# Optimization experiments

Measured on AMD Instinct MI355X. Metric: run time of the kernel, lower is better.

## Reference

```python
import jax, jax.numpy as jnp
import numpy as np

R = 5                       # kernels_radius
D = 2 * R + 1               # kernels_diameter
KERNELS_DESC = [
    {"weight": 0.9, "xy": 6.0, "image": 0.1},
    {"weight": 0.1, "xy": 6.0},
]


def _unfold(t, r):
    """torch F.unfold with padding=r, stride=1 -> [N, C, D, D, H, W]."""
    N, C, H, W = t.shape
    d = 2 * r + 1
    tp = jnp.pad(t, ((0, 0), (0, 0), (r, r), (r, r)))
    # fixed small loop over D*D kernel offsets (121), not over data dims
    pats = jnp.stack(
        [tp[:, :, i:i + H, j:j + W] for i in range(d) for j in range(d)],
        axis=2,
    )
    return pats.reshape(N, C, d, d, H, W)


def reference(x, y_hat):
    N, _, H, W = x.shape
    dt = x.dtype
    # xy coordinate feature [N, 2, H, W]: (col index, row index)
    cols = jnp.broadcast_to(jnp.arange(W, dtype=dt)[None, :], (H, W))
    rows = jnp.broadcast_to(jnp.arange(H, dtype=dt)[:, None], (H, W))
    xy = jnp.broadcast_to(jnp.stack([cols, rows], 0)[None], (N, 2, H, W))

    kernels = jnp.zeros((N, 1, D, D, H, W), dtype=dt)
    for desc in KERNELS_DESC:
        feats = []
        for modality, sigma in desc.items():
            if modality == 'weight':
                continue
            f = xy if modality == 'xy' else x
            feats.append(f / sigma)
        features = jnp.concatenate(feats, axis=1)          # [N, c, H, W]
        k = _unfold(features, R)                           # [N, c, D, D, H, W]
        k = k - k[:, :, R, R][:, :, None, None]            # diff to window center
        k = jnp.exp((-0.5 * k ** 2).sum(axis=1, keepdims=True))
        k = k.at[:, :, R, R].set(0.0)                      # zero self-affinity
        kernels = kernels + desc['weight'] * k

    Cy = y_hat.shape[1]
    yu = _unfold(y_hat, R)                                  # [N, Cy, D, D, H, W]
    prod = (kernels * yu).reshape(N, Cy, D * D, H, W).sum(axis=2)
    loss = kernels.sum() - (prod * y_hat).sum()
    denom = jnp.asarray(N * H * W, dtype=dt)
    return loss / denom


def setup_inputs() -> dict:
    key = jax.random.key(0)
    k1, k2 = jax.random.split(key)
    x = jax.random.normal(k1, (4, 3, 128, 128), dtype=jnp.float32)
    y_hat = jax.random.uniform(k2, (4, 21, 128, 128), dtype=jnp.float32)
    return {"x": x, "y_hat": y_hat}
```

## Files before the change

### kernel.cpp

```cpp
#include <hip/hip_runtime.h>

typedef _Float16 half2_t __attribute__((ext_vector_type(2)));

constexpr int IMG_H = 128;
constexpr int IMG_W = 128;
constexpr int N_IMG = 4;
constexpr int CXCH = 3;
constexpr int CYCH = 21;
constexpr int RAD = 5;
constexpr int DIA = 11;
constexpr int TILE_H = 8;
constexpr int TILE_W = 16;
constexpr int PT_H = TILE_H + 2 * RAD;
constexpr int PT_W = TILE_W + 2 * RAD;
constexpr int NPIX = PT_H * PT_W;
constexpr int NPIXT = TILE_H * TILE_W;
constexpr int NGROUP = 4;
constexpr int NTHREADS = NPIXT * NGROUP;
constexpr int NPAIR = 60;
constexpr int PPG = NPAIR / NGROUP;
constexpr int HW = IMG_H * IMG_W;
constexpr int SYW = 12;


__device__ __forceinline__ unsigned pkh(float a, float b) {
    half2_t h; h.x = (_Float16)a; h.y = (_Float16)b;
    unsigned u; __builtin_memcpy(&u, &h, 4); return u;
}
__device__ __forceinline__ half2_t uph(unsigned u) {
    half2_t h; __builtin_memcpy(&h, &u, 4); return h;
}
__device__ __forceinline__ float dot2(unsigned a, half2_t b, float c) {
#if __has_builtin(__builtin_amdgcn_fdot2)
    return __builtin_amdgcn_fdot2(uph(a), b, c, false);
#else
    half2_t ah = uph(a);
    return c + (float)ah.x * (float)b.x + (float)ah.y * (float)b.y;
#endif
}

__global__ __launch_bounds__(NTHREADS, 4)
void gcrf_kernel(const float* __restrict__ x, const float* __restrict__ y,
                 float* __restrict__ out) {
    __shared__ __align__(16) unsigned syh[NPIX * SYW];
    __shared__ int   s_pk[NPAIR];
    __shared__ float s_e1[NPAIR];
    __shared__ float s_red[NTHREADS / 64];

    const int tid = threadIdx.x;
    const int n = blockIdx.z;
    const int h0 = blockIdx.y * TILE_H;
    const int w0 = blockIdx.x * TILE_W;

    const float* xb = x + (size_t)n * CXCH * HW;
    const float* yb = y + (size_t)n * CYCH * HW;

    if (tid < NPAIR) {
        int di = tid < 5 ? 0 : 1 + (tid - 5) / 11;
        int dj = tid < 5 ? tid + 1 : (tid - 5) % 11 - 5;
        s_pk[tid] = (di << 8) | (dj + 8);
        s_e1[tid] = __expf(-0.5f * (float)(di * di + dj * dj) * (1.0f / 36.0f));
    }

    for (int p = tid; p < NPIX; p += NTHREADS) {
        int ti = p / PT_W, tj = p - ti * PT_W;
        int gh = h0 + ti - RAD, gw = w0 + tj - RAD;
        bool inb = ((unsigned)gh < (unsigned)IMG_H) && ((unsigned)gw < (unsigned)IMG_W);
        int gofs = gh * IMG_W + gw;
        float v[CYCH];
        #pragma unroll
        for (int c = 0; c < CYCH; c++) v[c] = inb ? yb[c * HW + gofs] : 0.0f;
        float xv[CXCH];
        #pragma unroll
        for (int c = 0; c < CXCH; c++) xv[c] = inb ? xb[c * HW + gofs] : 0.0f;
        unsigned d[SYW];
        #pragma unroll
        for (int q = 0; q < 10; q++) d[q] = pkh(v[2 * q], v[2 * q + 1]);
        d[10] = pkh(xv[0], xv[1]);
        d[11] = pkh(xv[2], v[20]);
        unsigned* dst = &syh[p * SYW];
        *(uint4*)&dst[0] = make_uint4(d[0], d[1], d[2], d[3]);
        *(uint4*)&dst[4] = make_uint4(d[4], d[5], d[6], d[7]);
        *(uint4*)&dst[8] = make_uint4(d[8], d[9], d[10], d[11]);
    }
    __syncthreads();

    const int g = tid >> 7;
    const int pix = tid & (NPIXT - 1);
    const int tx = pix & (TILE_W - 1);
    const int ty = pix >> 4;
    const int h = h0 + ty, w = w0 + tx;
    const int cp = (ty + RAD) * PT_W + (tx + RAD);
    const unsigned* base = &syh[cp * SYW];

    uint4 c0 = *(const uint4*)&base[0];
    uint4 c1 = *(const uint4*)&base[4];
    uint4 c2 = *(const uint4*)&base[8];
    half2_t yc[10];
    yc[0] = uph(c0.x); yc[1] = uph(c0.y); yc[2] = uph(c0.z); yc[3] = uph(c0.w);
    yc[4] = uph(c1.x); yc[5] = uph(c1.y); yc[6] = uph(c1.z); yc[7] = uph(c1.w);
    yc[8] = uph(c2.x); yc[9] = uph(c2.y);
    half2_t cxa = uph(c2.z), cxb = uph(c2.w);
    const float cx0 = (float)cxa.x, cx1 = (float)cxa.y;
    const float cx2 = (float)cxb.x, y20c = (float)cxb.y;

    float acc = 0.0f;
    if (g == 0) {
        int i0 = max(0, RAD - h), i1 = min(DIA - 1, IMG_H - 1 - h + RAD);
        int j0 = max(0, RAD - w), j1 = min(DIA - 1, IMG_W - 1 - w + RAD);
        int n_oob = DIA * DIA - (i1 - i0 + 1) * (j1 - j0 + 1);
        if (n_oob > 0) {
            float oxy = (float)(h * h + w * w) * (1.0f / 36.0f);
            float s2c = cx0 * cx0 + cx1 * cx1 + cx2 * cx2;
            float kvo = __expf(-0.5f * oxy) * (0.9f * __expf(-50.0f * s2c) + 0.1f);
            acc = (float)n_oob * kvo;
        }
    }

    int offs[PPG]; float e1v[PPG];
    #pragma unroll
    for (int t = 0; t < PPG; t++) {
        int k = g * PPG + t;
        int pk = s_pk[k];
        int di = pk >> 8, dj = (pk & 255) - 8;
        offs[t] = (di * PT_W + dj) * SYW;
        bool inb = (h + di < IMG_H) & ((unsigned)(w + dj) < (unsigned)IMG_W);
        e1v[t] = inb ? s_e1[k] : 0.0f;
    }

    float accp = 0.0f;
    #pragma unroll
    for (int t = 0; t < PPG; t++) {
        const unsigned* q = base + offs[t];
        uint4 a0 = *(const uint4*)&q[0];
        uint4 a1 = *(const uint4*)&q[4];
        uint4 a2 = *(const uint4*)&q[8];
        float dot = 0.0f;
        dot = dot2(a0.x, yc[0], dot); dot = dot2(a0.y, yc[1], dot);
        dot = dot2(a0.z, yc[2], dot); dot = dot2(a0.w, yc[3], dot);
        dot = dot2(a1.x, yc[4], dot); dot = dot2(a1.y, yc[5], dot);
        dot = dot2(a1.z, yc[6], dot); dot = dot2(a1.w, yc[7], dot);
        dot = dot2(a2.x, yc[8], dot); dot = dot2(a2.y, yc[9], dot);
        half2_t xq = uph(a2.z), xr = uph(a2.w);
        dot = fmaf((float)xr.y, y20c, dot);
        float d0 = (float)xq.x - cx0, d1 = (float)xq.y - cx1, d2 = (float)xr.x - cx2;
        float s2 = fmaf(d0, d0, fmaf(d1, d1, d2 * d2));
        float kv = e1v[t] * fmaf(0.9f, __expf(-50.0f * s2), 0.1f);
        accp = fmaf(kv, 1.0f - dot, accp);
    }

    float total = acc + 2.0f * accp;

    #pragma unroll
    for (int s = 32; s > 0; s >>= 1) total += __shfl_down(total, s, 64);
    if ((tid & 63) == 0) s_red[tid >> 6] = total;
    __syncthreads();
    if (tid == 0) {
        float bs = 0.0f;
        #pragma unroll
        for (int wv = 0; wv < NTHREADS / 64; wv++) bs += s_red[wv];
        atomicAdd(out, bs * (1.0f / (float)(N_IMG * HW)));
    }
}

extern "C" void kernel_launch(void* const* d_in, const int* in_sizes, int n_in,
                              void* d_out, int out_size, void* d_ws, size_t ws_size,
                              hipStream_t stream) {
    const float* x = (const float*)d_in[0];
    const float* y = (const float*)d_in[1];
    float* out = (float*)d_out;
    hipMemsetAsync(out, 0, sizeof(float), stream);
    dim3 grid(IMG_W / TILE_W, IMG_H / TILE_H, N_IMG);
    gcrf_kernel<<<grid, NTHREADS, 0, stream>>>(x, y, out);
}
```

Measured before the change: 78.17 us.

## Enlarge tiles to 16x16 with two pair groups and two-stage reduction

Doubles the tile height and halves the number of neighbor-pair groups per pixel, so each block loads relatively less halo into shared memory. The pair loop is split into chunks to limit live registers. The global atomic and memset are replaced by per-block partial sums written to workspace, reduced by a second single-block kernel. Fewer blocks may reduce occupancy across the GPU's compute units, and the extra kernel launch adds overhead.

```diff
diff --git a/kernel.cpp b/kernel.cpp
--- a/kernel.cpp
+++ b/kernel.cpp
@@ -9,18 +9,20 @@
 constexpr int CYCH = 21;
 constexpr int RAD = 5;
 constexpr int DIA = 11;
-constexpr int TILE_H = 8;
+constexpr int TILE_H = 16;
 constexpr int TILE_W = 16;
 constexpr int PT_H = TILE_H + 2 * RAD;
 constexpr int PT_W = TILE_W + 2 * RAD;
 constexpr int NPIX = PT_H * PT_W;
 constexpr int NPIXT = TILE_H * TILE_W;
-constexpr int NGROUP = 4;
+constexpr int NGROUP = 2;
 constexpr int NTHREADS = NPIXT * NGROUP;
 constexpr int NPAIR = 60;
 constexpr int PPG = NPAIR / NGROUP;
+constexpr int CHUNK = 15;
 constexpr int HW = IMG_H * IMG_W;
 constexpr int SYW = 12;
+constexpr int NBLK = (IMG_W / TILE_W) * (IMG_H / TILE_H) * N_IMG;
 
 
 __device__ __forceinline__ unsigned pkh(float a, float b) {
@@ -39,9 +41,9 @@
 #endif
 }
 
-__global__ __launch_bounds__(NTHREADS, 4)
+__global__ __launch_bounds__(NTHREADS, 2)
 void gcrf_kernel(const float* __restrict__ x, const float* __restrict__ y,
-                 float* __restrict__ out) {
+                 float* __restrict__ partials) {
     __shared__ __align__(16) unsigned syh[NPIX * SYW];
     __shared__ int   s_pk[NPAIR];
     __shared__ float s_e1[NPAIR];
@@ -85,7 +87,7 @@
     }
     __syncthreads();
 
-    const int g = tid >> 7;
+    const int g = tid >> 8;
     const int pix = tid & (NPIXT - 1);
     const int tx = pix & (TILE_W - 1);
     const int ty = pix >> 4;
@@ -117,36 +119,39 @@
         }
     }
 
-    int offs[PPG]; float e1v[PPG];
-    #pragma unroll
-    for (int t = 0; t < PPG; t++) {
-        int k = g * PPG + t;
-        int pk = s_pk[k];
-        int di = pk >> 8, dj = (pk & 255) - 8;
-        offs[t] = (di * PT_W + dj) * SYW;
-        bool inb = (h + di < IMG_H) & ((unsigned)(w + dj) < (unsigned)IMG_W);
-        e1v[t] = inb ? s_e1[k] : 0.0f;
-    }
-
     float accp = 0.0f;
     #pragma unroll
-    for (int t = 0; t < PPG; t++) {
-        const unsigned* q = base + offs[t];
-        uint4 a0 = *(const uint4*)&q[0];
-        uint4 a1 = *(const uint4*)&q[4];
-        uint4 a2 = *(const uint4*)&q[8];
-        float dot = 0.0f;
-        dot = dot2(a0.x, yc[0], dot); dot = dot2(a0.y, yc[1], dot);
-        dot = dot2(a0.z, yc[2], dot); dot = dot2(a0.w, yc[3], dot);
-        dot = dot2(a1.x, yc[4], dot); dot = dot2(a1.y, yc[5], dot);
-        dot = dot2(a1.z, yc[6], dot); dot = dot2(a1.w, yc[7], dot);
-        dot = dot2(a2.x, yc[8], dot); dot = dot2(a2.y, yc[9], dot);
-        half2_t xq = uph(a2.z), xr = uph(a2.w);
-        dot = fmaf((float)xr.y, y20c, dot);
-        float d0 = (float)xq.x - cx0, d1 = (float)xq.y - cx1, d2 = (float)xr.x - cx2;
-        float s2 = fmaf(d0, d0, fmaf(d1, d1, d2 * d2));
-        float kv = e1v[t] * fmaf(0.9f, __expf(-50.0f * s2), 0.1f);
-        accp = fmaf(kv, 1.0f - dot, accp);
+    for (int ch = 0; ch < PPG / CHUNK; ch++) {
+        int offs[CHUNK]; float e1v[CHUNK];
+        #pragma unroll
+        for (int t = 0; t < CHUNK; t++) {
+            int k = g * PPG + ch * CHUNK + t;
+            int pk = s_pk[k];
+            int di = pk >> 8, dj = (pk & 255) - 8;
+            offs[t] = (di * PT_W + dj) * SYW;
+            bool inb = (h + di < IMG_H) & ((unsigned)(w + dj) < (unsigned)IMG_W);
+            e1v[t] = inb ? s_e1[k] : 0.0f;
+        }
+        #pragma unroll
+        for (int t = 0; t < CHUNK; t++) {
+            const unsigned* q = base + offs[t];
+            uint4 a0 = *(const uint4*)&q[0];
+            uint4 a1 = *(const uint4*)&q[4];
+            uint4 a2 = *(const uint4*)&q[8];
+            float dot = 0.0f;
+            dot = dot2(a0.x, yc[0], dot); dot = dot2(a0.y, yc[1], dot);
+            dot = dot2(a0.z, yc[2], dot); dot = dot2(a0.w, yc[3], dot);
+            dot = dot2(a1.x, yc[4], dot); dot = dot2(a1.y, yc[5], dot);
+            dot = dot2(a1.z, yc[6], dot); dot = dot2(a1.w, yc[7], dot);
+            dot = dot2(a2.x, yc[8], dot); dot = dot2(a2.y, yc[9], dot);
+            half2_t xq = uph(a2.z), xr = uph(a2.w);
+            dot = fmaf((float)xr.y, y20c, dot);
+            float d0 = (float)xq.x - cx0, d1 = (float)xq.y - cx1,
+                  d2 = (float)xr.x - cx2;
+            float s2 = fmaf(d0, d0, fmaf(d1, d1, d2 * d2));
+            float kv = e1v[t] * fmaf(0.9f, __expf(-50.0f * s2), 0.1f);
+            accp = fmaf(kv, 1.0f - dot, accp);
+        }
     }
 
     float total = acc + 2.0f * accp;
@@ -159,7 +164,25 @@
         float bs = 0.0f;
         #pragma unroll
         for (int wv = 0; wv < NTHREADS / 64; wv++) bs += s_red[wv];
-        atomicAdd(out, bs * (1.0f / (float)(N_IMG * HW)));
+        int blk = (blockIdx.z * gridDim.y + blockIdx.y) * gridDim.x + blockIdx.x;
+        partials[blk] = bs;
+    }
+}
+
+__global__ __launch_bounds__(NBLK)
+void gcrf_sum(const float* __restrict__ partials, float* __restrict__ out) {
+    __shared__ float s_red[NBLK / 64];
+    int tid = threadIdx.x;
+    float v = partials[tid];
+    #pragma unroll
+    for (int s = 32; s > 0; s >>= 1) v += __shfl_down(v, s, 64);
+    if ((tid & 63) == 0) s_red[tid >> 6] = v;
+    __syncthreads();
+    if (tid == 0) {
+        float bs = 0.0f;
+        #pragma unroll
+        for (int wv = 0; wv < NBLK / 64; wv++) bs += s_red[wv];
+        out[0] = bs * (1.0f / (float)(N_IMG * HW));
     }
 }
 
@@ -169,7 +192,8 @@
     const float* x = (const float*)d_in[0];
     const float* y = (const float*)d_in[1];
     float* out = (float*)d_out;
-    hipMemsetAsync(out, 0, sizeof(float), stream);
+    float* partials = (float*)d_ws;
     dim3 grid(IMG_W / TILE_W, IMG_H / TILE_H, N_IMG);
-    gcrf_kernel<<<grid, NTHREADS, 0, stream>>>(x, y, out);
+    gcrf_kernel<<<grid, NTHREADS, 0, stream>>>(x, y, partials);
+    gcrf_sum<<<1, NBLK, 0, stream>>>(partials, out);
 }
```

Result: slower. 83.07 us (+6.3%).
